# Kernel optimization log

Hardware: AMD Instinct MI355X
Metric: run time of the kernel (lower is better)

Reference implementation:

```python
import jax, jax.numpy as jnp
import numpy as np

EPS = 1e-5
K = 27  # 3x3x3 kernel taps


def conv3d(x, w, b):
    # x: [B,C,D,H,W], w: [O,I,3,3,3], SAME padding == pad 1, stride 1
    out = jax.lax.conv_general_dilated(
        x, w, window_strides=(1, 1, 1), padding='SAME',
        dimension_numbers=('NCDHW', 'OIDHW', 'NCDHW'))
    return out + b.reshape(1, -1, 1, 1, 1)


def batchnorm(x, gamma, beta):
    # training-mode BN over (B,D,H,W), matching nn.BatchNorm3d in train()
    m = x.mean(axis=(0, 2, 3, 4), keepdims=True)
    v = x.var(axis=(0, 2, 3, 4), keepdims=True)
    return (x - m) * jax.lax.rsqrt(v + EPS) * gamma.reshape(1, -1, 1, 1, 1) + beta.reshape(1, -1, 1, 1, 1)


def trilinear_gather(xg, pd, ph, pw):
    # xg: [cpg,D,H,W]; pd/ph/pw: [K,D,H,W] float sample positions.
    # Zero-padding outside the volume (invalid corners contribute 0).
    D, H, W = xg.shape[1], xg.shape[2], xg.shape[3]
    d0, h0, w0 = jnp.floor(pd), jnp.floor(ph), jnp.floor(pw)
    fd, fh, fw = pd - d0, ph - h0, pw - w0
    out = jnp.zeros((xg.shape[0],) + pd.shape, xg.dtype)
    for dd in (0, 1):
        for hh in (0, 1):
            for ww in (0, 1):
                d_, h_, w_ = d0 + dd, h0 + hh, w0 + ww
                wt = ((fd if dd else 1.0 - fd)
                      * (fh if hh else 1.0 - fh)
                      * (fw if ww else 1.0 - fw))
                valid = ((d_ >= 0) & (d_ < D) & (h_ >= 0) & (h_ < H)
                         & (w_ >= 0) & (w_ < W))
                di = jnp.clip(d_, 0, D - 1).astype(jnp.int32)
                hi = jnp.clip(h_, 0, H - 1).astype(jnp.int32)
                wi = jnp.clip(w_, 0, W - 1).astype(jnp.int32)
                vals = xg[:, di, hi, wi]  # [cpg,K,D,H,W]
                out = out + vals * (wt * valid)[None]
    return out


def deform_conv3d(x, off, w, G, cpg):
    # x: [B,C,D,H,W]; off: [B,G*K*3,D,H,W]; w: [O,C,3,3,3]
    B, C, D, H, W = x.shape
    k = jnp.arange(K)
    kd = (k // 9 - 1).astype(x.dtype)
    kh = (k // 3 % 3 - 1).astype(x.dtype)
    kw = (k % 3 - 1).astype(x.dtype)
    off = off.reshape(B, G, K, 3, D, H, W)
    pd = off[:, :, :, 0] + kd[:, None, None, None] + jnp.arange(D, dtype=x.dtype)[:, None, None]
    ph = off[:, :, :, 1] + kh[:, None, None, None] + jnp.arange(H, dtype=x.dtype)[:, None]
    pw = off[:, :, :, 2] + kw[:, None, None, None] + jnp.arange(W, dtype=x.dtype)
    xg = x.reshape(B, G, cpg, D, H, W)
    gather = jax.vmap(jax.vmap(trilinear_gather))  # over B, then G
    cols = gather(xg, pd, ph, pw)  # [B,G,cpg,K,D,H,W]
    wg = w.reshape(w.shape[0], G, cpg, K)
    return jnp.einsum('bgckdhw,ogck->bodhw', cols, wg)


def setup_inputs() -> dict:
    key = jax.random.key(0)
    B, C, D, H, W = 2, 64, 8, 56, 56
    cpg = 8
    G = C // cpg
    OFFC = G * 3 * K  # 648
    ks = jax.random.split(key, 12)
    inp = {
        'x': jax.random.normal(ks[0], (B, C, D, H, W), jnp.float32),
        'w_off1': jax.random.normal(ks[1], (OFFC, C, 3, 3, 3), jnp.float32) * 0.01,
        'b_off1': jax.random.normal(ks[2], (OFFC,), jnp.float32) * 0.01,
        'w_dc1': jax.random.normal(ks[3], (C, C, 3, 3, 3), jnp.float32) * 0.05,
        'gamma1': jnp.ones((C,), jnp.float32),
        'beta1': jnp.zeros((C,), jnp.float32),
        'w_off2': jax.random.normal(ks[4], (OFFC, C, 3, 3, 3), jnp.float32) * 0.01,
        'b_off2': jax.random.normal(ks[5], (OFFC,), jnp.float32) * 0.01,
        'w_dc2': jax.random.normal(ks[6], (C, C, 3, 3, 3), jnp.float32) * 0.05,
        'gamma2': jnp.ones((C,), jnp.float32),
        'beta2': jnp.zeros((C,), jnp.float32),
    }
    return inp


def reference(x, w_off1, b_off1, w_dc1, gamma1, beta1,
              w_off2, b_off2, w_dc2, gamma2, beta2):
    cpg = 8
    G = x.shape[1] // cpg
    residual = x
    off = conv3d(x, w_off1, b_off1)
    h = deform_conv3d(x, off, w_dc1, G, cpg)
    h = jax.nn.relu(batchnorm(h, gamma1, beta1))
    off = conv3d(h, w_off2, b_off2)
    h = deform_conv3d(h, off, w_dc2, G, cpg)
    h = batchnorm(h, gamma2, beta2)
    return jax.nn.relu(h + residual)
```

## Files before the change

kernel.cpp:

```cpp
#include <hip/hip_runtime.h>

#define B_    2
#define C_    64
#define D_    8
#define H_    56
#define W_    56
#define HW_   3136
#define DHW_  25088
#define G_    8
#define K_    27
#define OFFC_ 648

#define PD_   10
#define PH_   58
#define PW_   58
#define PSPAT (PD_ * PH_ * PW_)
#define PGSZ  (PSPAT * 8)

#define PACKB ((B_ * G_ * PSPAT + 255) / 256)
#define TG1   ((OFFC_ * 2048) / 256)
#define TG2   ((C_ * 1728) / 256)

typedef __attribute__((ext_vector_type(8))) short  bf16x8;
typedef __attribute__((ext_vector_type(4))) float  f32x4;
typedef __attribute__((ext_vector_type(8))) unsigned short ushort8;

__device__ __forceinline__ unsigned short f2bf(float f) {
    unsigned u = __float_as_uint(f);
    u = (u + 0x7FFFu + ((u >> 16) & 1u)) >> 16;
    return (unsigned short)u;
}
__device__ __forceinline__ float bf2f(unsigned short u) {
    return __uint_as_float(((unsigned)u) << 16);
}
__device__ __forceinline__ unsigned cvt_pk_bf16(float lo, float hi) {
    unsigned r;
    asm("v_cvt_pk_bf16_f32 %0, %1, %2" : "=v"(r) : "v"(lo), "v"(hi));
    return r;
}
__device__ __forceinline__ void gload_lds16(const void* g, void* l) {
    __builtin_amdgcn_global_load_lds(
        (const __attribute__((address_space(1))) unsigned int*)g,
        (__attribute__((address_space(3))) unsigned int*)l, 16, 0, 0);
}

__global__ __launch_bounds__(256) void prep_kernel(
    const float* __restrict__ x, unsigned short* __restrict__ xp, int npack,
    const float* __restrict__ woff, unsigned short* __restrict__ wT2,
    const float* __restrict__ wdc, unsigned short* __restrict__ wdcT)
{
    int blk = blockIdx.x;
    const int t = threadIdx.x;
    if (blk < npack) {
        int i = blk * 256 + t;
        if (i >= B_ * G_ * PSPAT) return;
        int b = i / (G_ * PSPAT);
        int rem = i - b * G_ * PSPAT;
        int g = rem / PSPAT, s = rem - g * PSPAT;
        int dp = s / (PH_ * PW_), r2 = s - dp * (PH_ * PW_);
        int hp = r2 / PW_, wp = r2 - hp * PW_;
        ushort8 v = {0, 0, 0, 0, 0, 0, 0, 0};
        if (dp >= 1 && dp <= D_ && hp >= 1 && hp <= H_ && wp >= 1 && wp <= W_) {
            const float* src = x + (size_t)(b * C_ + g * 8) * DHW_ + (dp - 1) * HW_ + (hp - 1) * W_ + (wp - 1);
            #pragma unroll
            for (int c = 0; c < 8; ++c) v[c] = f2bf(src[c * DHW_]);
        }
        *(ushort8*)(xp + (size_t)i * 8) = v;
        return;
    }
    blk -= npack;
    if (blk < TG1) {
        int i = blk * 256 + t;
        int oc = i >> 11, r = i & 2047;
        int g = r >> 8, r2 = r & 255;
        int s = r2 >> 3, c = r2 & 7;
        int tap = s ^ (oc & 7);
        unsigned short v = 0;
        if (tap < 27) v = f2bf(woff[(size_t)oc * 1728 + (g * 8 + c) * 27 + tap]);
        wT2[i] = v;
        return;
    }
    blk -= TG1;
    {
        int i = blk * 256 + t;
        int oc = i / 1728, k = i - oc * 1728;
        int icc = k / 216, r = k - icc * 216;
        int tap = r >> 3, icl = r & 7;
        wdcT[i] = f2bf(wdc[(size_t)oc * 1728 + (icc * 8 + icl) * 27 + tap]);
    }
}

#define CROW 512
__device__ __forceinline__ int swz(int row, int kByte) {
    return row * CROW + (kByte ^ ((row & 7) << 4));
}

#define XRH 12
__global__ __launch_bounds__(256, 2) void conv_off_mfma_kernel(
    const unsigned short* __restrict__ xpad, const unsigned short* __restrict__ wT2,
    const float* __restrict__ bias, unsigned short* __restrict__ out)
{
    __shared__ __align__(16) char wb[64 * CROW];
    __shared__ __align__(16) unsigned short xr[3 * XRH * 64 * 8];

    const int oc0  = blockIdx.x * 64;
    const int pos0 = blockIdx.y * 512;
    const int b    = blockIdx.z >> 3;
    const int d    = blockIdx.z & 7;
    const int h0   = pos0 / 56;
    const int t    = threadIdx.x;
    const int lane = t & 63;
    const int li   = lane & 15;
    const int ts   = lane >> 4;
    const int wv   = t >> 6;

    int poff[8];
    #pragma unroll
    for (int pb = 0; pb < 8; ++pb) {
        int p  = pos0 + wv * 128 + pb * 16 + li;
        int pc = p < HW_ ? p : HW_ - 1;
        int hp = pc / 56, wp = pc - hp * 56;
        poff[pb] = (hp - h0) * 64 + wp;
    }
    int offk[7];
    #pragma unroll
    for (int kk = 0; kk < 7; ++kk) {
        int tap = min(4 * kk + ts, 26);
        int dd = tap / 9, hh = (tap / 3) % 3, ww = tap - (tap / 3) * 3;
        offk[kk] = (dd * XRH + hh) * 64 + ww;
    }

    int xsrc[9];
    #pragma unroll
    for (int it = 0; it < 9; ++it) {
        int i = it * 256 + t;
        int w = i & 63, rest = i >> 6;
        int hl = rest % XRH, dd = rest / XRH;
        int dp = d + dd;
        int hp = min(h0 + hl, PH_ - 1);
        int wp = min(w, PW_ - 1);
        xsrc[it] = ((dp * PH_ + hp) * PW_ + wp) * 8;
    }
    size_t wsrc[8];
    #pragma unroll
    for (int it = 0; it < 8; ++it) {
        int j = it * 256 + t;
        int rowg = min(oc0 + (j >> 5), OFFC_ - 1);
        wsrc[it] = ((size_t)rowg * 8) * 256 + (size_t)(j & 31) * 8;
    }

    f32x4 acc[4][8];
    #pragma unroll
    for (int i = 0; i < 4; ++i)
        #pragma unroll
        for (int j = 0; j < 8; ++j) acc[i][j] = (f32x4){0.f, 0.f, 0.f, 0.f};

    const unsigned short* xb0 = xpad + (size_t)(b * 8) * PGSZ;

    for (int g = 0; g < 8; ++g) {
        __syncthreads();
        const unsigned short* xb = xb0 + (size_t)g * PGSZ;
        #pragma unroll
        for (int it = 0; it < 9; ++it)
            gload_lds16(xb + xsrc[it], &xr[(it * 256 + t) * 8]);
        const unsigned short* wg = wT2 + (size_t)g * 256;
        #pragma unroll
        for (int it = 0; it < 8; ++it)
            gload_lds16(wg + wsrc[it], wb + (size_t)(it * 256 + t) * 16);
        __syncthreads();

        #pragma unroll
        for (int kk = 0; kk < 7; ++kk) {
            int tap = 4 * kk + ts;
            bf16x8 a[4];
            #pragma unroll
            for (int oa = 0; oa < 4; ++oa)
                a[oa] = *(const bf16x8*)(wb + swz(oa * 16 + li, tap * 16));
            #pragma unroll
            for (int pb = 0; pb < 8; ++pb) {
                bf16x8 bfrag = *(const bf16x8*)&xr[(offk[kk] + poff[pb]) * 8];
                #pragma unroll
                for (int oa = 0; oa < 4; ++oa)
                    acc[oa][pb] = __builtin_amdgcn_mfma_f32_16x16x32_bf16(a[oa], bfrag, acc[oa][pb], 0, 0, 0);
            }
        }
    }

    #pragma unroll
    for (int oa = 0; oa < 4; ++oa)
        #pragma unroll
        for (int pb = 0; pb < 8; ++pb)
            #pragma unroll
            for (int r = 0; r < 4; ++r) {
                int ocg = oc0 + oa * 16 + ts * 4 + r;
                int p   = pos0 + wv * 128 + pb * 16 + li;
                if (ocg < OFFC_ && p < HW_)
                    out[((size_t)(b * OFFC_ + ocg) * 8 + d) * HW_ + p] = f2bf(acc[oa][pb][r] + bias[ocg]);
            }
}

#define REDS 17
__global__ __launch_bounds__(256, 4) void deform_mfma_kernel(
    const unsigned short* __restrict__ xpad, const unsigned short* __restrict__ off,
    const unsigned short* __restrict__ wT, float* __restrict__ hout,
    float* __restrict__ hpart)
{
    __shared__ float red[3 * 64 * REDS];

    const int id   = blockIdx.y * 196 + blockIdx.x;
    const int sid  = (id & 7) * 784 + (id >> 3);
    const int pt   = sid % 196;
    const int rest = sid / 196;
    const int bd   = rest >> 1;
    const int gs   = rest & 1;
    const int b    = bd >> 3;
    const int d    = bd & 7;
    const int pos0 = pt * 16;

    const int t    = threadIdx.x;
    const int lane = t & 63;
    const int li   = lane & 15, ts = lane >> 4;
    const int wv   = t >> 6;
    const int g    = gs * 4 + wv;

    const int p  = pos0 + li;
    const int hq = p / 56, wq = p - hq * 56;

    f32x4 acc[4];
    #pragma unroll
    for (int i = 0; i < 4; ++i) acc[i] = (f32x4){0.f, 0.f, 0.f, 0.f};

    {
        const unsigned short* xg = xpad + (size_t)(b * 8 + g) * PGSZ;
        const unsigned short* wg = wT + g * 216;
        #pragma unroll
        for (int kk = 0; kk < 7; ++kk) {
            int tap = 4 * kk + ts;
            int tc  = tap < 27 ? tap : 26;
            bf16x8 afr[4];
            #pragma unroll
            for (int oa = 0; oa < 4; ++oa)
                afr[oa] = *(const bf16x8*)(wg + (size_t)(oa * 16 + li) * 1728 + tc * 8);
            bf16x8 bfr;
            {
                float a8[8] = {0.f, 0.f, 0.f, 0.f, 0.f, 0.f, 0.f, 0.f};
                if (tap < 27) {
                    int kd = tap / 9 - 1, kh = (tap / 3) % 3 - 1, kw = tap - (tap / 3) * 3 - 1;
                    size_t ob = ((size_t)(b * OFFC_ + (g * 27 + tap) * 3) * 8 + d) * HW_ + p;
                    float pd = bf2f(off[ob])            + (float)(kd + d);
                    float ph = bf2f(off[ob + DHW_])     + (float)(kh + hq);
                    float pw = bf2f(off[ob + 2 * DHW_]) + (float)(kw + wq);
                    float fd0 = floorf(pd), fh0 = floorf(ph), fw0 = floorf(pw);
                    float fd = pd - fd0, fh = ph - fh0, fw = pw - fw0;
                    int d0 = (int)fd0, h0i = (int)fh0, w0i = (int)fw0;
                    #pragma unroll
                    for (int tp = 0; tp < 8; ++tp) {
                        int dd = tp >> 2, hh = (tp >> 1) & 1, ww = tp & 1;
                        int di = d0 + dd, hi = h0i + hh, wi = w0i + ww;
                        float wgt = (dd ? fd : 1.f - fd) * (hh ? fh : 1.f - fh) * (ww ? fw : 1.f - fw);
                        bool valid = ((unsigned)di < 8u) && ((unsigned)hi < 56u) && ((unsigned)wi < 56u);
                        wgt = valid ? wgt : 0.f;
                        int dc = valid ? di : 0, hc = valid ? hi : 0, wc = valid ? wi : 0;
                        ushort8 v = *(const ushort8*)(xg + (((size_t)(dc + 1) * PH_ + hc + 1) * PW_ + wc + 1) * 8);
                        #pragma unroll
                        for (int c = 0; c < 8; ++c) a8[c] += bf2f(v[c]) * wgt;
                    }
                }
                union { unsigned u[4]; bf16x8 v; } cv;
                #pragma unroll
                for (int c = 0; c < 4; ++c) cv.u[c] = cvt_pk_bf16(a8[2 * c], a8[2 * c + 1]);
                bfr = cv.v;
            }
            #pragma unroll
            for (int oa = 0; oa < 4; ++oa)
                acc[oa] = __builtin_amdgcn_mfma_f32_16x16x32_bf16(afr[oa], bfr, acc[oa], 0, 0, 0);
        }
    }

    if (wv > 0) {
        float* rr = red + (wv - 1) * 64 * REDS + lane * REDS;
        #pragma unroll
        for (int oa = 0; oa < 4; ++oa)
            #pragma unroll
            for (int q = 0; q < 4; ++q)
                rr[oa * 4 + q] = acc[oa][q];
    }
    __syncthreads();
    if (wv == 0) {
        #pragma unroll
        for (int w2 = 0; w2 < 3; ++w2) {
            const float* rr = red + w2 * 64 * REDS + lane * REDS;
            #pragma unroll
            for (int oa = 0; oa < 4; ++oa)
                #pragma unroll
                for (int q = 0; q < 4; ++q)
                    acc[oa][q] += rr[oa * 4 + q];
        }
        float* dst = gs ? hpart : hout;
        #pragma unroll
        for (int oa = 0; oa < 4; ++oa)
            #pragma unroll
            for (int r = 0; r < 4; ++r) {
                int oc = oa * 16 + ts * 4 + r;
                dst[((size_t)(b * C_ + oc) * 8 + d) * HW_ + p] = acc[oa][r];
            }
    }
}

__global__ __launch_bounds__(256) void bn_stats_partial_kernel(
    const float* __restrict__ ha, const float* __restrict__ hb, float* __restrict__ part)
{
    const int c = blockIdx.x, s = blockIdx.y;
    const int t = threadIdx.x;
    const int SL = (B_ * DHW_) / 16;
    float sum = 0.f, sq = 0.f;
    for (int j = s * SL + t * 4; j < (s + 1) * SL; j += 1024) {
        int b = j / DHW_, i = j - b * DHW_;
        size_t base = (size_t)(b * C_ + c) * DHW_ + i;
        f32x4 va = *(const f32x4*)(ha + base);
        f32x4 vb = *(const f32x4*)(hb + base);
        #pragma unroll
        for (int q = 0; q < 4; ++q) { float v = va[q] + vb[q]; sum += v; sq += v * v; }
    }
    #pragma unroll
    for (int o = 32; o > 0; o >>= 1) {
        sum += __shfl_down(sum, o);
        sq  += __shfl_down(sq, o);
    }
    __shared__ float rs[4], rq[4];
    if ((t & 63) == 0) { rs[t >> 6] = sum; rq[t >> 6] = sq; }
    __syncthreads();
    if (t == 0) {
        part[c * 16 + s]        = rs[0] + rs[1] + rs[2] + rs[3];
        part[1024 + c * 16 + s] = rq[0] + rq[1] + rq[2] + rq[3];
    }
}

__global__ void bn_stats_finalize_kernel(
    const float* __restrict__ part, float* __restrict__ stats)
{
    int c = threadIdx.x;
    if (c >= 64) return;
    float s = 0.f, q = 0.f;
    for (int i = 0; i < 16; ++i) { s += part[c * 16 + i]; q += part[1024 + c * 16 + i]; }
    float inv = 1.f / (float)(B_ * DHW_);
    float m   = s * inv;
    float var = q * inv - m * m;
    stats[c]      = m;
    stats[C_ + c] = rsqrtf(fmaxf(var, 0.f) + 1e-5f);
}

__global__ __launch_bounds__(256) void bn_relu_pack_kernel(
    const float* __restrict__ ha, const float* __restrict__ hb,
    const float* __restrict__ stats,
    const float* __restrict__ gamma, const float* __restrict__ beta,
    unsigned short* __restrict__ out)
{
    int i = blockIdx.x * 256 + threadIdx.x;
    if (i >= B_ * G_ * PSPAT) return;
    int b = i / (G_ * PSPAT);
    int rem = i - b * G_ * PSPAT;
    int g = rem / PSPAT, s = rem - g * PSPAT;
    int dp = s / (PH_ * PW_), r2 = s - dp * (PH_ * PW_);
    int hp = r2 / PW_, wp = r2 - hp * PW_;
    ushort8 o8 = {0, 0, 0, 0, 0, 0, 0, 0};
    if (dp >= 1 && dp <= D_ && hp >= 1 && hp <= H_ && wp >= 1 && wp <= W_) {
        int dhw = (dp - 1) * HW_ + (hp - 1) * W_ + (wp - 1);
        #pragma unroll
        for (int c = 0; c < 8; ++c) {
            int ch = g * 8 + c;
            size_t base = (size_t)(b * C_ + ch) * DHW_ + dhw;
            float v = (ha[base] + hb[base] - stats[ch]) * stats[C_ + ch] * gamma[ch] + beta[ch];
            o8[c] = f2bf(v > 0.f ? v : 0.f);
        }
    }
    *(ushort8*)(out + (size_t)i * 8) = o8;
}

__global__ __launch_bounds__(256) void bn_add_relu_kernel(
    float* __restrict__ hbuf, const float* __restrict__ hpart,
    const float* __restrict__ xres, const float* __restrict__ stats,
    const float* __restrict__ gamma, const float* __restrict__ beta)
{
    const int n = B_ * C_ * DHW_;
    for (int i = blockIdx.x * 256 + threadIdx.x; i < n; i += gridDim.x * 256) {
        int c = (i / DHW_) & (C_ - 1);
        float v = (hbuf[i] + hpart[i] - stats[c]) * stats[C_ + c] * gamma[c] + beta[c] + xres[i];
        hbuf[i] = v > 0.f ? v : 0.f;
    }
}

extern "C" void kernel_launch(void* const* d_in, const int* in_sizes, int n_in,
                              void* d_out, int out_size, void* d_ws, size_t ws_size,
                              hipStream_t stream)
{
    const float* x      = (const float*)d_in[0];
    const float* w_off1 = (const float*)d_in[1];
    const float* b_off1 = (const float*)d_in[2];
    const float* w_dc1  = (const float*)d_in[3];
    const float* gamma1 = (const float*)d_in[4];
    const float* beta1  = (const float*)d_in[5];
    const float* w_off2 = (const float*)d_in[6];
    const float* b_off2 = (const float*)d_in[7];
    const float* w_dc2  = (const float*)d_in[8];
    const float* gamma2 = (const float*)d_in[9];
    const float* beta2  = (const float*)d_in[10];
    float* out = (float*)d_out;

    unsigned short* offb = (unsigned short*)d_ws;
    unsigned short* xpad = offb + (size_t)B_ * OFFC_ * DHW_;
    unsigned short* h1pd = xpad + (size_t)B_ * G_ * PGSZ;
    unsigned short* wT2  = h1pd + (size_t)B_ * G_ * PGSZ;
    unsigned short* wdcT = wT2  + (size_t)OFFC_ * 2048;
    float* h1raw = (float*)(wdcT + (size_t)C_ * 1728);
    float* hpart = h1raw + (size_t)B_ * C_ * DHW_;
    float* stats = hpart + (size_t)B_ * C_ * DHW_;
    float* part  = stats + 128;

    dim3 cgrid(11, 7, B_ * D_);
    dim3 dgrid(196, 32);
    dim3 sgrid(C_, 16);

    prep_kernel             <<<PACKB + TG1 + TG2, 256, 0, stream>>>(x, xpad, PACKB, w_off1, wT2, w_dc1, wdcT);
    conv_off_mfma_kernel    <<<cgrid, 256, 0, stream>>>(xpad, wT2, b_off1, offb);
    deform_mfma_kernel      <<<dgrid, 256, 0, stream>>>(xpad, offb, wdcT, h1raw, hpart);
    bn_stats_partial_kernel <<<sgrid, 256, 0, stream>>>(h1raw, hpart, part);
    bn_stats_finalize_kernel<<<1, 64, 0, stream>>>(part, stats);
    bn_relu_pack_kernel     <<<PACKB, 256, 0, stream>>>(h1raw, hpart, stats, gamma1, beta1, h1pd);

    prep_kernel             <<<TG1 + TG2, 256, 0, stream>>>(nullptr, nullptr, 0, w_off2, wT2, w_dc2, wdcT);
    conv_off_mfma_kernel    <<<cgrid, 256, 0, stream>>>(h1pd, wT2, b_off2, offb);
    deform_mfma_kernel      <<<dgrid, 256, 0, stream>>>(h1pd, offb, wdcT, out, hpart);
    bn_stats_partial_kernel <<<sgrid, 256, 0, stream>>>(out, hpart, part);
    bn_stats_finalize_kernel<<<1, 64, 0, stream>>>(part, stats);
    bn_add_relu_kernel      <<<1024, 256, 0, stream>>>(out, hpart, x, stats, gamma2, beta2);
}
```

Baseline: 660.9 us.

## Double-buffer LDS in offset conv and use 512-thread blocks

Reworks the offset-conv kernel to double-buffer both the input tile and the weight tile in shared memory. The next group's global-to-LDS loads are issued before the current group's MFMA work, which removes one barrier per group and hides load latency. Blocks grow to 512 threads (8 waves), each wave covering 64 positions instead of 128, so per-wave accumulators halve. The cost is double the LDS footprint, which drops occupancy to one block per CU, plus a few extra clamped loads for the padded slot.

New measurement: 639.8 us. -3.2%, faster.

```diff
diff --git a/kernel.cpp b/kernel.cpp
--- a/kernel.cpp
+++ b/kernel.cpp
@@ -96,12 +96,13 @@
 }
 
 #define XRH 12
-__global__ __launch_bounds__(256, 2) void conv_off_mfma_kernel(
+#define XSLOT 2560
+__global__ __launch_bounds__(512, 1) void conv_off_mfma_kernel(
     const unsigned short* __restrict__ xpad, const unsigned short* __restrict__ wT2,
     const float* __restrict__ bias, unsigned short* __restrict__ out)
 {
-    __shared__ __align__(16) char wb[64 * CROW];
-    __shared__ __align__(16) unsigned short xr[3 * XRH * 64 * 8];
+    __shared__ __align__(16) unsigned short xr[2][XSLOT * 8];
+    __shared__ __align__(16) char wb[2][64 * CROW];
 
     const int oc0  = blockIdx.x * 64;
     const int pos0 = blockIdx.y * 512;
@@ -114,10 +115,10 @@
     const int ts   = lane >> 4;
     const int wv   = t >> 6;
 
-    int poff[8];
-    #pragma unroll
-    for (int pb = 0; pb < 8; ++pb) {
-        int p  = pos0 + wv * 128 + pb * 16 + li;
+    int poff[4];
+    #pragma unroll
+    for (int pb = 0; pb < 4; ++pb) {
+        int p  = pos0 + wv * 64 + pb * 16 + li;
         int pc = p < HW_ ? p : HW_ - 1;
         int hp = pc / 56, wp = pc - hp * 56;
         poff[pb] = (hp - h0) * 64 + wp;
@@ -130,70 +131,80 @@
         offk[kk] = (dd * XRH + hh) * 64 + ww;
     }
 
-    int xsrc[9];
-    #pragma unroll
-    for (int it = 0; it < 9; ++it) {
-        int i = it * 256 + t;
+    int xsrc[5];
+    #pragma unroll
+    for (int it = 0; it < 5; ++it) {
+        int i = it * 512 + t;
         int w = i & 63, rest = i >> 6;
-        int hl = rest % XRH, dd = rest / XRH;
-        int dp = d + dd;
+        int hl = rest % XRH;
+        int dd = min(rest / XRH, 2);
+        int dp = min(d + dd, PD_ - 1);
         int hp = min(h0 + hl, PH_ - 1);
         int wp = min(w, PW_ - 1);
         xsrc[it] = ((dp * PH_ + hp) * PW_ + wp) * 8;
     }
-    size_t wsrc[8];
-    #pragma unroll
-    for (int it = 0; it < 8; ++it) {
-        int j = it * 256 + t;
+    size_t wsrc[4];
+    #pragma unroll
+    for (int it = 0; it < 4; ++it) {
+        int j = it * 512 + t;
         int rowg = min(oc0 + (j >> 5), OFFC_ - 1);
         wsrc[it] = ((size_t)rowg * 8) * 256 + (size_t)(j & 31) * 8;
     }
 
-    f32x4 acc[4][8];
+    f32x4 acc[4][4];
     #pragma unroll
     for (int i = 0; i < 4; ++i)
         #pragma unroll
-        for (int j = 0; j < 8; ++j) acc[i][j] = (f32x4){0.f, 0.f, 0.f, 0.f};
+        for (int j = 0; j < 4; ++j) acc[i][j] = (f32x4){0.f, 0.f, 0.f, 0.f};
 
     const unsigned short* xb0 = xpad + (size_t)(b * 8) * PGSZ;
 
+    #pragma unroll
+    for (int it = 0; it < 5; ++it)
+        gload_lds16(xb0 + xsrc[it], &xr[0][(it * 512 + t) * 8]);
+    #pragma unroll
+    for (int it = 0; it < 4; ++it)
+        gload_lds16(wT2 + wsrc[it], wb[0] + (size_t)(it * 512 + t) * 16);
+    __syncthreads();
+
     for (int g = 0; g < 8; ++g) {
-        __syncthreads();
-        const unsigned short* xb = xb0 + (size_t)g * PGSZ;
-        #pragma unroll
-        for (int it = 0; it < 9; ++it)
-            gload_lds16(xb + xsrc[it], &xr[(it * 256 + t) * 8]);
-        const unsigned short* wg = wT2 + (size_t)g * 256;
-        #pragma unroll
-        for (int it = 0; it < 8; ++it)
-            gload_lds16(wg + wsrc[it], wb + (size_t)(it * 256 + t) * 16);
-        __syncthreads();
-
+        const int cur = g & 1;
+        if (g < 7) {
+            const unsigned short* xb = xb0 + (size_t)(g + 1) * PGSZ;
+            const unsigned short* wg = wT2 + (size_t)(g + 1) * 256;
+            #pragma unroll
+            for (int it = 0; it < 5; ++it)
+                gload_lds16(xb + xsrc[it], &xr[cur ^ 1][(it * 512 + t) * 8]);
+            #pragma unroll
+            for (int it = 0; it < 4; ++it)
+                gload_lds16(wg + wsrc[it], wb[cur ^ 1] + (size_t)(it * 512 + t) * 16);
+        }
         #pragma unroll
         for (int kk = 0; kk < 7; ++kk) {
             int tap = 4 * kk + ts;
             bf16x8 a[4];
             #pragma unroll
             for (int oa = 0; oa < 4; ++oa)
-                a[oa] = *(const bf16x8*)(wb + swz(oa * 16 + li, tap * 16));
-            #pragma unroll
-            for (int pb = 0; pb < 8; ++pb) {
-                bf16x8 bfrag = *(const bf16x8*)&xr[(offk[kk] + poff[pb]) * 8];
+                a[oa] = *(const bf16x8*)(wb[cur] + swz(oa * 16 + li, tap * 16));
+            #pragma unroll
+            for (int pb = 0; pb < 4; ++pb) {
+                bf16x8 bfrag = *(const bf16x8*)&xr[cur][(offk[kk] + poff[pb]) * 8];
                 #pragma unroll
                 for (int oa = 0; oa < 4; ++oa)
                     acc[oa][pb] = __builtin_amdgcn_mfma_f32_16x16x32_bf16(a[oa], bfrag, acc[oa][pb], 0, 0, 0);
             }
         }
+        __syncthreads();
     }
 
     #pragma unroll
     for (int oa = 0; oa < 4; ++oa)
         #pragma unroll
-        for (int pb = 0; pb < 8; ++pb)
+        for (int pb = 0; pb < 4; ++pb)
             #pragma unroll
             for (int r = 0; r < 4; ++r) {
                 int ocg = oc0 + oa * 16 + ts * 4 + r;
-                int p   = pos0 + wv * 128 + pb * 16 + li;
+                int p   = pos0 + wv * 64 + pb * 16 + li;
                 if (ocg < OFFC_ && p < HW_)
                     out[((size_t)(b * OFFC_ + ocg) * 8 + d) * HW_ + p] = f2bf(acc[oa][pb][r] + bias[ocg]);
             }
@@ -422,14 +433,14 @@
     dim3 sgrid(C_, 16);
 
     prep_kernel             <<<PACKB + TG1 + TG2, 256, 0, stream>>>(x, xpad, PACKB, w_off1, wT2, w_dc1, wdcT);
-    conv_off_mfma_kernel    <<<cgrid, 256, 0, stream>>>(xpad, wT2, b_off1, offb);
+    conv_off_mfma_kernel    <<<cgrid, 512, 0, stream>>>(xpad, wT2, b_off1, offb);
     deform_mfma_kernel      <<<dgrid, 256, 0, stream>>>(xpad, offb, wdcT, h1raw, hpart);
     bn_stats_partial_kernel <<<sgrid, 256, 0, stream>>>(h1raw, hpart, part);
     bn_stats_finalize_kernel<<<1, 64, 0, stream>>>(part, stats);
     bn_relu_pack_kernel     <<<PACKB, 256, 0, stream>>>(h1raw, hpart, stats, gamma1, beta1, h1pd);
 
     prep_kernel             <<<TG1 + TG2, 256, 0, stream>>>(nullptr, nullptr, 0, w_off2, wT2, w_dc2, wdcT);
-    conv_off_mfma_kernel    <<<cgrid, 256, 0, stream>>>(h1pd, wT2, b_off2, offb);
+    conv_off_mfma_kernel    <<<cgrid, 512, 0, stream>>>(h1pd, wT2, b_off2, offb);
     deform_mfma_kernel      <<<dgrid, 256, 0, stream>>>(h1pd, offb, wdcT, out, hpart);
     bn_stats_partial_kernel <<<sgrid, 256, 0, stream>>>(out, hpart, part);
     bn_stats_finalize_kernel<<<1, 64, 0, stream>>>(part, stats);
```
